# Performance work log

Measured on AMD Instinct MI355X. Metric: run time of the kernel, lower is better.

## Reference

```python
import jax, jax.numpy as jnp
import numpy as np

B, L, H, E, R = 2, 512, 768, 512, 32768
H2 = H // 2


def setup_inputs() -> dict:
    key = jax.random.key(0)
    ks = jax.random.split(key, 16)
    s = 0.02
    inp = {
        "hidden_states": jax.random.normal(ks[0], (B, L, H), dtype=jnp.float32),
        "ent_start": jax.random.randint(ks[1], (B, E), 0, L, dtype=jnp.int32),
        "ent_label": jax.random.randint(ks[2], (B, E), 0, 3, dtype=jnp.int32),
        "rel_head": jax.random.randint(ks[3], (B, R), 0, E, dtype=jnp.int32),
        "rel_tail": jax.random.randint(ks[4], (B, R), 0, E, dtype=jnp.int32),
        "rel_label": jax.random.randint(ks[5], (B, R), 0, 2, dtype=jnp.int32),
        "entity_emb": jax.random.normal(ks[6], (3, H), dtype=jnp.float32) * s,
        "head_W1": jax.random.normal(ks[7], (2 * H, H), dtype=jnp.float32) * s,
        "head_b1": jnp.zeros((H,), dtype=jnp.float32),
        "head_W2": jax.random.normal(ks[8], (H, H2), dtype=jnp.float32) * s,
        "head_b2": jnp.zeros((H2,), dtype=jnp.float32),
        "tail_W1": jax.random.normal(ks[9], (2 * H, H), dtype=jnp.float32) * s,
        "tail_b1": jnp.zeros((H,), dtype=jnp.float32),
        "tail_W2": jax.random.normal(ks[10], (H, H2), dtype=jnp.float32) * s,
        "tail_b2": jnp.zeros((H2,), dtype=jnp.float32),
        "bil_W": jax.random.normal(ks[11], (2, H2, H2), dtype=jnp.float32) * s,
        "lin_W": jax.random.normal(ks[12], (2 * H2, 2), dtype=jnp.float32) * s,
        "lin_b": jnp.zeros((2,), dtype=jnp.float32),
    }
    return inp


def _mlp(x, W1, b1, W2, b2):
    # Linear -> ReLU -> (dropout=identity) -> Linear -> ReLU -> (dropout=identity)
    h = jax.nn.relu(jnp.einsum("brd,dh->brh", x, W1) + b1)
    return jax.nn.relu(jnp.einsum("brh,hk->brk", h, W2) + b2)


def reference(hidden_states, ent_start, ent_label, rel_head, rel_tail, rel_label,
              entity_emb, head_W1, head_b1, head_W2, head_b2,
              tail_W1, tail_b1, tail_W2, tail_b2, bil_W, lin_W, lin_b):
    # Gather entity start token index and label for each relation endpoint
    h_idx = jnp.take_along_axis(ent_start, rel_head, axis=1)  # [B,R]
    t_idx = jnp.take_along_axis(ent_start, rel_tail, axis=1)
    h_lab = jnp.take_along_axis(ent_label, rel_head, axis=1)
    t_lab = jnp.take_along_axis(ent_label, rel_tail, axis=1)

    # Gather hidden states at entity start positions: [B,R,H]
    h_tok = jnp.take_along_axis(hidden_states, h_idx[..., None], axis=1)
    t_tok = jnp.take_along_axis(hidden_states, t_idx[..., None], axis=1)

    head_repr = jnp.concatenate([h_tok, entity_emb[h_lab]], axis=-1)  # [B,R,2H]
    tail_repr = jnp.concatenate([t_tok, entity_emb[t_lab]], axis=-1)

    heads = _mlp(head_repr, head_W1, head_b1, head_W2, head_b2)  # [B,R,H2]
    tails = _mlp(tail_repr, tail_W1, tail_b1, tail_W2, tail_b2)

    # BiaffineAttention: bilinear(x1,x2) + linear(cat(x1,x2))
    bil = jnp.einsum("brd,ode,bre->bro", heads, bil_W, tails)  # [B,R,2]
    lin = jnp.einsum("brc,co->bro", jnp.concatenate([heads, tails], axis=-1), lin_W) + lin_b
    logits = bil + lin  # [B,R,2]

    # Per-doc mean cross-entropy, summed over docs (matches loss accumulation)
    logp = jax.nn.log_softmax(logits, axis=-1)
    ce = -jnp.take_along_axis(logp, rel_label[..., None], axis=-1)[..., 0]  # [B,R]
    loss = ce.mean(axis=-1).sum()

    return loss, logits.reshape(B * R, 2)
```

## Files before the change

kernel.cpp:

```cpp
#include <hip/hip_runtime.h>
#include <math.h>

#define BB 2
#define LL 512
#define HH 768
#define EE 512
#define RR 32768
#define H2 384
#define MM 1024

typedef __attribute__((ext_vector_type(8))) short     bf16x8;
typedef __attribute__((ext_vector_type(4))) float     f32x4;
typedef __attribute__((ext_vector_type(8))) unsigned short u16x8;

#define BUFE (64 * 72)

__device__ __forceinline__ unsigned short f2bf(float f) {
    unsigned int u = __float_as_uint(f);
    u = (u + 0x7FFFu + ((u >> 16) & 1u)) >> 16;
    return (unsigned short)u;
}

__device__ __forceinline__ void wtrans(const float* __restrict__ src,
                                       unsigned short* __restrict__ dst,
                                       int K, int N, int tile, unsigned short* T)
{
    const int t = threadIdx.x;
    const int tn = N >> 5;
    const int n0 = (tile % tn) * 32;
    const int k0 = (tile / tn) * 32;
    const int r  = t >> 3;
    const int c4 = (t & 7) * 4;
    const float4 g = *(const float4*)(src + (size_t)(k0 + r) * N + n0 + c4);
    T[(c4 + 0) * 40 + r] = f2bf(g.x);
    T[(c4 + 1) * 40 + r] = f2bf(g.y);
    T[(c4 + 2) * 40 + r] = f2bf(g.z);
    T[(c4 + 3) * 40 + r] = f2bf(g.w);
    __syncthreads();
    const int n  = t >> 3;
    const int k4 = (t & 7) * 4;
    *(ushort4*)(dst + (size_t)(n0 + n) * K + k0 + k4) = *(ushort4*)&T[n * 40 + k4];
}

__global__ __launch_bounds__(256) void prep(
    const float* __restrict__ hW1, const float* __restrict__ tW1,
    unsigned short* __restrict__ W1ht, unsigned short* __restrict__ W1tt,
    const float* __restrict__ hidden, const int* __restrict__ ent_start,
    const float* __restrict__ emb,
    const float* __restrict__ hb1, const float* __restrict__ tb1,
    unsigned short* __restrict__ Hbf, float* __restrict__ embc,
    float* __restrict__ hlin, float* __restrict__ tlin, float* __restrict__ out)
{
    __shared__ unsigned short T[32 * 40];
    __shared__ float red[4][192];
    const int bid = blockIdx.x;
    const int t = threadIdx.x;

    if (bid == 2200) {
        const float4 z = {0.f, 0.f, 0.f, 0.f};
        ((float4*)hlin)[t] = z; ((float4*)hlin)[256 + t] = z;
        ((float4*)tlin)[t] = z; ((float4*)tlin)[256 + t] = z;
        if (t == 0) out[0] = 0.f;
        return;
    }

    if (bid >= 2176) {
        const int eb = bid - 2176;
        const int tc = t & 63;
        const int kg = t >> 6;
        const int n = eb * 64 + tc;
        const float* W = (n < 768) ? hW1 : tW1;
        const int cc = (n < 768) ? n : n - 768;
        float a0 = 0.f, a1 = 0.f, a2 = 0.f;
        const int kbeg = kg * 192;
        #pragma unroll 8
        for (int k = kbeg; k < kbeg + 192; ++k) {
            const float w = W[(size_t)(768 + k) * 768 + cc];
            a0 += emb[k] * w;
            a1 += emb[768 + k] * w;
            a2 += emb[1536 + k] * w;
        }
        red[kg][0 * 64 + tc] = a0;
        red[kg][1 * 64 + tc] = a1;
        red[kg][2 * 64 + tc] = a2;
        __syncthreads();
        if (kg == 0) {
            const float b = (n < 768) ? hb1[n] : tb1[n - 768];
            #pragma unroll
            for (int l = 0; l < 3; ++l) {
                embc[l * 1536 + n] = b + red[0][l * 64 + tc] + red[1][l * 64 + tc]
                                       + red[2][l * 64 + tc] + red[3][l * 64 + tc];
            }
        }
        return;
    }

    if (bid >= 1152) {
        const int m = bid - 1152;
        if (t >= 96) return;
        const int b = m >> 9;
        const int idx = ent_start[m];
        const float4* s = (const float4*)(hidden + (size_t)(b * LL + idx) * HH);
        const float4 v0 = s[2 * t];
        const float4 v1 = s[2 * t + 1];
        u16x8 o;
        o[0] = f2bf(v0.x); o[1] = f2bf(v0.y); o[2] = f2bf(v0.z); o[3] = f2bf(v0.w);
        o[4] = f2bf(v1.x); o[5] = f2bf(v1.y); o[6] = f2bf(v1.z); o[7] = f2bf(v1.w);
        *(u16x8*)(Hbf + (size_t)m * 768 + 8 * t) = o;
        return;
    }

    if (bid < 576) wtrans(hW1, W1ht, 768, 768, bid, T);
    else           wtrans(tW1, W1tt, 768, 768, bid - 576, T);
}

template<bool RELU, bool BIAS, bool EB, bool WBF16, bool LIN>
__device__ __forceinline__ void gemm_body(
    int tile, int nx,
    const unsigned short* __restrict__ A, int lda, int aoff1,
    const unsigned short* __restrict__ Bt0, const unsigned short* __restrict__ Bt1,
    int ldb, int Nh,
    const float* __restrict__ bias0, const float* __restrict__ bias1,
    const float* __restrict__ embc, const int* __restrict__ labels,
    const float* __restrict__ linW, float* __restrict__ hlin, float* __restrict__ tlin,
    int K, unsigned short* __restrict__ Cb, int ldc,
    unsigned short* As, unsigned short* Bs)
{
    const int tid = threadIdx.x;
    const int n0 = (tile % nx) * 64;
    const int m0 = (tile / nx) * 64;
    const int hf = (n0 >= Nh) ? 1 : 0;
    const unsigned short* Bt = hf ? Bt1 : Bt0;
    const int nc0 = n0 - (hf ? Nh : 0);
    const int aoff = hf ? aoff1 : 0;

    const int sr = tid >> 2;
    const int sk = (tid & 3) * 16;

    const unsigned short* Ap = A + (size_t)(m0 + sr) * lda + aoff + sk;
    const unsigned short* Bp = Bt + (size_t)(nc0 + sr) * ldb + sk;

    const int lane = tid & 63;
    const int wave = tid >> 6;
    const int wm = (wave & 1) * 32;
    const int wn = (wave >> 1) * 32;
    const int l15 = lane & 15;
    const int quad = lane >> 4;
    const int swo = sr * 72 + sk;
    const int aro = quad * 8;

    f32x4 acc00 = {}, acc01 = {}, acc10 = {}, acc11 = {};

    u16x8 pa0, pa1, pb0, pb1;
    u16x8 qa0, qa1, qb0, qb1;

#define GLOADP(ko) { pa0 = *(const u16x8*)(Ap + (ko)); pa1 = *(const u16x8*)(Ap + (ko) + 8); \
                     pb0 = *(const u16x8*)(Bp + (ko)); pb1 = *(const u16x8*)(Bp + (ko) + 8); }
#define GLOADQ(ko) { qa0 = *(const u16x8*)(Ap + (ko)); qa1 = *(const u16x8*)(Ap + (ko) + 8); \
                     qb0 = *(const u16x8*)(Bp + (ko)); qb1 = *(const u16x8*)(Bp + (ko) + 8); }
#define SWRITEP(bi) { unsigned short* Aw = As + (bi) * BUFE; unsigned short* Bw = Bs + (bi) * BUFE; \
                      *(u16x8*)&Aw[swo] = pa0; *(u16x8*)&Aw[swo + 8] = pa1; \
                      *(u16x8*)&Bw[swo] = pb0; *(u16x8*)&Bw[swo + 8] = pb1; }
#define SWRITEQ(bi) { unsigned short* Aw = As + (bi) * BUFE; unsigned short* Bw = Bs + (bi) * BUFE; \
                      *(u16x8*)&Aw[swo] = qa0; *(u16x8*)&Aw[swo + 8] = qa1; \
                      *(u16x8*)&Bw[swo] = qb0; *(u16x8*)&Bw[swo + 8] = qb1; }
#define BAR() { asm volatile("s_waitcnt lgkmcnt(0)" ::: "memory"); \
                __builtin_amdgcn_s_barrier(); \
                __builtin_amdgcn_sched_barrier(0); }
#define MFMA8(bi) { const unsigned short* Ac = As + (bi) * BUFE; \
                    const unsigned short* Bc = Bs + (bi) * BUFE; \
        const bf16x8 fa0 = *(const bf16x8*)&Ac[(wm + l15) * 72 + aro]; \
        const bf16x8 fa1 = *(const bf16x8*)&Ac[(wm + 16 + l15) * 72 + aro]; \
        const bf16x8 fb0 = *(const bf16x8*)&Bc[(wn + l15) * 72 + aro]; \
        const bf16x8 fb1 = *(const bf16x8*)&Bc[(wn + 16 + l15) * 72 + aro]; \
        const bf16x8 ga0 = *(const bf16x8*)&Ac[(wm + l15) * 72 + aro + 32]; \
        const bf16x8 ga1 = *(const bf16x8*)&Ac[(wm + 16 + l15) * 72 + aro + 32]; \
        const bf16x8 gb0 = *(const bf16x8*)&Bc[(wn + l15) * 72 + aro + 32]; \
        const bf16x8 gb1 = *(const bf16x8*)&Bc[(wn + 16 + l15) * 72 + aro + 32]; \
        acc00 = __builtin_amdgcn_mfma_f32_16x16x32_bf16(fa0, fb0, acc00, 0, 0, 0); \
        acc01 = __builtin_amdgcn_mfma_f32_16x16x32_bf16(fa0, fb1, acc01, 0, 0, 0); \
        acc10 = __builtin_amdgcn_mfma_f32_16x16x32_bf16(fa1, fb0, acc10, 0, 0, 0); \
        acc11 = __builtin_amdgcn_mfma_f32_16x16x32_bf16(fa1, fb1, acc11, 0, 0, 0); \
        acc00 = __builtin_amdgcn_mfma_f32_16x16x32_bf16(ga0, gb0, acc00, 0, 0, 0); \
        acc01 = __builtin_amdgcn_mfma_f32_16x16x32_bf16(ga0, gb1, acc01, 0, 0, 0); \
        acc10 = __builtin_amdgcn_mfma_f32_16x16x32_bf16(ga1, gb0, acc10, 0, 0, 0); \
        acc11 = __builtin_amdgcn_mfma_f32_16x16x32_bf16(ga1, gb1, acc11, 0, 0, 0); }

    const int NT = K >> 6;

    GLOADP(0);
    GLOADQ(64);
    SWRITEP(0);

    for (int it = 0; it < NT; it += 2) {
        BAR();
        if (it + 2 < NT) GLOADP((it + 2) << 6);
        MFMA8(0);
        SWRITEQ(1);
        BAR();
        if (it + 3 < NT) GLOADQ((it + 3) << 6);
        MFMA8(1);
        if (it + 2 < NT) SWRITEP(0);
    }

#undef GLOADP
#undef GLOADQ
#undef SWRITEP
#undef SWRITEQ
#undef BAR
#undef MFMA8

    float bias_v0 = 0.f, bias_v1 = 0.f;
    if (BIAS) {
        const float* bb = hf ? bias1 : bias0;
        bias_v0 = bb[nc0 + wn + l15];
        bias_v1 = bb[nc0 + wn + 16 + l15];
    }
    const int col0 = n0 + wn + l15;
    const int col1 = col0 + 16;
    float2 lw0 = {0.f, 0.f}, lw1 = {0.f, 0.f};
    float* lout = nullptr;
    if (LIN) {
        lw0 = ((const float2*)linW)[col0];
        lw1 = ((const float2*)linW)[col1];
        lout = hf ? tlin : hlin;
    }
    const f32x4 accs[2][2] = {{acc00, acc01}, {acc10, acc11}};
    #pragma unroll
    for (int mi = 0; mi < 2; ++mi) {
        #pragma unroll
        for (int r = 0; r < 4; ++r) {
            const int row = m0 + wm + mi * 16 + quad * 4 + r;
            float v0 = accs[mi][0][r];
            float v1 = accs[mi][1][r];
            if (BIAS) { v0 += bias_v0; v1 += bias_v1; }
            if (EB) {
                const int lab = labels[row];
                v0 += embc[lab * 1536 + col0];
                v1 += embc[lab * 1536 + col1];
            }
            if (RELU) { v0 = fmaxf(v0, 0.f); v1 = fmaxf(v1, 0.f); }
            if (WBF16) {
                Cb[(size_t)row * ldc + col0] = f2bf(v0);
                Cb[(size_t)row * ldc + col1] = f2bf(v1);
            }
            if (LIN) {
                float s0 = v0 * lw0.x + v1 * lw1.x;
                float s1 = v0 * lw0.y + v1 * lw1.y;
                #pragma unroll
                for (int o = 8; o >= 1; o >>= 1) {
                    s0 += __shfl_xor(s0, o, 64);
                    s1 += __shfl_xor(s1, o, 64);
                }
                if (l15 == 0) {
                    atomicAdd(&lout[2 * row],     s0);
                    atomicAdd(&lout[2 * row + 1], s1);
                }
            }
        }
    }
}

template<bool RELU, bool BIAS, bool EB, bool WBF16, bool LIN>
__global__ __launch_bounds__(256) void gemm_mfma(
    const unsigned short* __restrict__ A, int lda, int aoff1,
    const unsigned short* __restrict__ Bt0, const unsigned short* __restrict__ Bt1,
    int ldb, int Nh,
    const float* __restrict__ bias0, const float* __restrict__ bias1,
    const float* __restrict__ embc, const int* __restrict__ labels,
    const float* __restrict__ linW, float* __restrict__ hlin, float* __restrict__ tlin,
    int K, unsigned short* __restrict__ Cb, int ldc)
{
    __shared__ __align__(16) unsigned short As[2 * BUFE];
    __shared__ __align__(16) unsigned short Bs[2 * BUFE];
    gemm_body<RELU, BIAS, EB, WBF16, LIN>(
        blockIdx.y * gridDim.x + blockIdx.x, gridDim.x,
        A, lda, aoff1, Bt0, Bt1, ldb, Nh,
        bias0, bias1, embc, labels, linW, hlin, tlin,
        K, Cb, ldc, As, Bs);
}

__global__ __launch_bounds__(256) void gemm1_plus(
    const unsigned short* __restrict__ Hbf,
    const unsigned short* __restrict__ W1ht, const unsigned short* __restrict__ W1tt,
    const float* __restrict__ embc, const int* __restrict__ ent_label,
    unsigned short* __restrict__ Y1bf,
    const float* __restrict__ hW2, const float* __restrict__ tW2,
    const float* __restrict__ bilW,
    unsigned short* __restrict__ W2ht, unsigned short* __restrict__ W2tt,
    unsigned short* __restrict__ bW0t, unsigned short* __restrict__ bW1t,
    const int* __restrict__ rel_head, const int* __restrict__ rel_tail,
    const int* __restrict__ rel_label,
    int* __restrict__ counts2, unsigned* __restrict__ bins)
{
    __shared__ __align__(16) unsigned short As[2 * BUFE];
    __shared__ __align__(16) unsigned short Bs[2 * BUFE];
    const int bid = blockIdx.x;
    if (bid >= 1248) {
        __shared__ int lcnt[128];
        const int tid = threadIdx.x;
        const int blk = bid - 1248;
        const int batch = blk >> 5;
        const int blkb = blk & 31;
        if (tid < 128) lcnt[tid] = 0;
        __syncthreads();
        const int base = blk * 1024;
        #pragma unroll
        for (int k = 0; k < 4; ++k) {
            const int j = base + k * 256 + tid;
            const int h = rel_head[j];
            const int t = rel_tail[j];
            const int lab = rel_label[j];
            const int lbin = ((h >> 6) << 4) | (t >> 5);
            const int slot = atomicAdd(&lcnt[lbin], 1);
            const int gbin = (batch << 7) | lbin;
            bins[(gbin << 10) | (blkb << 5) | slot] =
                (unsigned)j | ((unsigned)lab << 17) |
                ((unsigned)(h & 63) << 18) | ((unsigned)(t & 31) << 24);
        }
        __syncthreads();
        if (tid < 128)
            counts2[(((batch << 7) | tid) << 5) | blkb] = lcnt[tid];
        return;
    }
    if (bid >= 384) {
        const int task = bid - 384;
        if (task < 288)      wtrans(hW2, W2ht, 768, 384, task, As);
        else if (task < 576) wtrans(tW2, W2tt, 768, 384, task - 288, As);
        else if (task < 720) wtrans(bilW, bW0t, 384, 384, task - 576, As);
        else                 wtrans(bilW + 384 * 384, bW1t, 384, 384, task - 720, As);
        return;
    }
    gemm_body<true, false, true, true, false>(
        bid, 24, Hbf, 768, 0, W1ht, W1tt, 768, 768,
        nullptr, nullptr, embc, ent_label, nullptr, nullptr, nullptr,
        768, Y1bf, 1536, As, Bs);
}

__global__ __launch_bounds__(256) void score_rel(
    const unsigned short* __restrict__ hWbf, const unsigned short* __restrict__ HTbf,
    const float* __restrict__ hlin, const float* __restrict__ tlin,
    const float* __restrict__ lin_b,
    const int* __restrict__ counts2, const unsigned* __restrict__ bins,
    float* __restrict__ out)
{
    __shared__ __align__(16) unsigned short As[2][64 * 72];
    __shared__ __align__(16) unsigned short Bs[2][32 * 72];
    __shared__ float wsum[4];
    __shared__ int cbuf[32];

    const int tid = threadIdx.x;
    const int t0 = blockIdx.x * 32;
    const int m0 = blockIdx.y * 64;
    const int batch = m0 >> 9;

    const int asr = tid >> 2;
    const int ask = (tid & 3) * 16;
    const unsigned short* Ap = hWbf + (size_t)(m0 + asr) * 768 + ask;
    const int bsr = tid >> 3;
    const int bsk = (tid & 7) * 8;
    const unsigned short* Bp = HTbf + (size_t)(batch * 512 + t0 + bsr) * 768 + 384 + bsk;

    const int lane = tid & 63;
    const int wave = tid >> 6;
    const int wm = (wave & 1) * 32;
    const int wn = (wave >> 1) * 16;
    const int l15 = lane & 15;
    const int quad = lane >> 4;
    const int aro = quad * 8;
    const int aswo = asr * 72 + ask;
    const int bswo = bsr * 72 + bsk;

    f32x4 p00 = {}, p01 = {};
    f32x4 p10 = {}, p11 = {};

#define KOA(it) (((it) < 6) ? (it) * 64 : ((it) - 6) * 64 + 384)
#define KOB(it) ((((it) < 6) ? (it) : (it) - 6) * 64)

    u16x8 pa0, pa1, pbv;
    u16x8 qa0, qa1, qbv;

#define SGLOADP(it) { pa0 = *(const u16x8*)(Ap + KOA(it)); pa1 = *(const u16x8*)(Ap + KOA(it) + 8); \
                      pbv = *(const u16x8*)(Bp + KOB(it)); }
#define SGLOADQ(it) { qa0 = *(const u16x8*)(Ap + KOA(it)); qa1 = *(const u16x8*)(Ap + KOA(it) + 8); \
                      qbv = *(const u16x8*)(Bp + KOB(it)); }
#define SSWRITEP(bi) { *(u16x8*)&As[bi][aswo] = pa0; *(u16x8*)&As[bi][aswo + 8] = pa1; \
                       *(u16x8*)&Bs[bi][bswo] = pbv; }
#define SSWRITEQ(bi) { *(u16x8*)&As[bi][aswo] = qa0; *(u16x8*)&As[bi][aswo + 8] = qa1; \
                       *(u16x8*)&Bs[bi][bswo] = qbv; }
#define SBAR() { asm volatile("s_waitcnt lgkmcnt(0)" ::: "memory"); \
                 __builtin_amdgcn_s_barrier(); \
                 __builtin_amdgcn_sched_barrier(0); }
#define SMFMA(bi, it) { \
        const unsigned short* Ac = As[bi]; \
        const unsigned short* Bc = Bs[bi]; \
        const bf16x8 fa0 = *(const bf16x8*)&Ac[(wm + l15) * 72 + aro]; \
        const bf16x8 fa1 = *(const bf16x8*)&Ac[(wm + 16 + l15) * 72 + aro]; \
        const bf16x8 fb  = *(const bf16x8*)&Bc[(wn + l15) * 72 + aro]; \
        const bf16x8 ga0 = *(const bf16x8*)&Ac[(wm + l15) * 72 + aro + 32]; \
        const bf16x8 ga1 = *(const bf16x8*)&Ac[(wm + 16 + l15) * 72 + aro + 32]; \
        const bf16x8 gb  = *(const bf16x8*)&Bc[(wn + l15) * 72 + aro + 32]; \
        if ((it) < 6) { \
            p00 = __builtin_amdgcn_mfma_f32_16x16x32_bf16(fa0, fb, p00, 0, 0, 0); \
            p01 = __builtin_amdgcn_mfma_f32_16x16x32_bf16(fa1, fb, p01, 0, 0, 0); \
            p00 = __builtin_amdgcn_mfma_f32_16x16x32_bf16(ga0, gb, p00, 0, 0, 0); \
            p01 = __builtin_amdgcn_mfma_f32_16x16x32_bf16(ga1, gb, p01, 0, 0, 0); \
        } else { \
            p10 = __builtin_amdgcn_mfma_f32_16x16x32_bf16(fa0, fb, p10, 0, 0, 0); \
            p11 = __builtin_amdgcn_mfma_f32_16x16x32_bf16(fa1, fb, p11, 0, 0, 0); \
            p10 = __builtin_amdgcn_mfma_f32_16x16x32_bf16(ga0, gb, p10, 0, 0, 0); \
            p11 = __builtin_amdgcn_mfma_f32_16x16x32_bf16(ga1, gb, p11, 0, 0, 0); \
        } }

    SGLOADP(0);
    SGLOADQ(1);
    SSWRITEP(0);

    #pragma unroll
    for (int it = 0; it < 12; it += 2) {
        SBAR();
        if (it + 2 < 12) SGLOADP(it + 2);
        SMFMA(0, it);
        SSWRITEQ(1);
        SBAR();
        if (it + 3 < 12) SGLOADQ(it + 3);
        SMFMA(1, it + 1);
        if (it + 2 < 12) SSWRITEP(0);
    }

#undef KOA
#undef KOB
#undef SGLOADP
#undef SGLOADQ
#undef SSWRITEP
#undef SSWRITEQ
#undef SBAR
#undef SMFMA

    __syncthreads();
    float* Sl = (float*)&As[0][0];
    const int col = wn + l15;
    #pragma unroll
    for (int mi = 0; mi < 2; ++mi) {
        #pragma unroll
        for (int r = 0; r < 4; ++r) {
            const int row = wm + mi * 16 + quad * 4 + r;
            Sl[row * 33 + col]           = mi ? p01[r] : p00[r];
            Sl[64 * 33 + row * 33 + col] = mi ? p11[r] : p10[r];
        }
    }
    const int bin = (batch << 7) | (((m0 >> 6) & 7) << 4) | (t0 >> 5);
    if (tid < 32) cbuf[tid] = counts2[(bin << 5) | tid];
    __syncthreads();

    const unsigned* mybins = bins + (bin << 10);
    const float lb0 = lin_b[0], lb1 = lin_b[1];
    float ce = 0.f;
    #pragma unroll
    for (int k = 0; k < 4; ++k) {
        const int si = k * 256 + tid;
        const int blkb = si >> 5;
        const int slot = si & 31;
        if (slot < cbuf[blkb]) {
            const unsigned rec = mybins[si];
            const int j   = rec & 0x1FFFF;
            const int lab = (rec >> 17) & 1;
            const int h6  = (rec >> 18) & 63;
            const int t5  = (rec >> 24) & 31;
            const int mh = m0 + h6;
            const int mt = batch * 512 + t0 + t5;
            const float2 hl = ((const float2*)hlin)[mh];
            const float2 tl = ((const float2*)tlin)[mt];
            const int so = h6 * 33 + t5;
            const float z0 = Sl[so]           + hl.x + tl.x + lb0;
            const float z1 = Sl[64 * 33 + so] + hl.y + tl.y + lb1;
            out[1 + 2 * (size_t)j] = z0;
            out[2 + 2 * (size_t)j] = z1;
            const float mx = fmaxf(z0, z1);
            const float mn = fminf(z0, z1);
            ce += mx + log1pf(expf(mn - mx)) - (lab ? z1 : z0);
        }
    }
    #pragma unroll
    for (int o = 32; o >= 1; o >>= 1) ce += __shfl_xor(ce, o, 64);
    if (lane == 0) wsum[wave] = ce;
    __syncthreads();
    if (tid == 0)
        atomicAdd(out, (wsum[0] + wsum[1] + wsum[2] + wsum[3]) * (1.0f / (float)RR));
}

extern "C" void kernel_launch(void* const* d_in, const int* in_sizes, int n_in,
                              void* d_out, int out_size, void* d_ws, size_t ws_size,
                              hipStream_t stream) {
    const float* hidden    = (const float*)d_in[0];
    const int*   ent_start = (const int*)d_in[1];
    const int*   ent_label = (const int*)d_in[2];
    const int*   rel_head  = (const int*)d_in[3];
    const int*   rel_tail  = (const int*)d_in[4];
    const int*   rel_label = (const int*)d_in[5];
    const float* emb       = (const float*)d_in[6];
    const float* head_W1   = (const float*)d_in[7];
    const float* head_b1   = (const float*)d_in[8];
    const float* head_W2   = (const float*)d_in[9];
    const float* head_b2   = (const float*)d_in[10];
    const float* tail_W1   = (const float*)d_in[11];
    const float* tail_b1   = (const float*)d_in[12];
    const float* tail_W2   = (const float*)d_in[13];
    const float* tail_b2   = (const float*)d_in[14];
    const float* bil_W     = (const float*)d_in[15];
    const float* lin_W     = (const float*)d_in[16];
    const float* lin_b     = (const float*)d_in[17];
    float* out = (float*)d_out;

    char* w = (char*)d_ws;
    auto carve = [&](size_t bytes) {
        char* p = w; w += (bytes + 255) & ~(size_t)255; return p;
    };
    unsigned short* Hbf  = (unsigned short*)carve((size_t)MM * 768 * 2);
    unsigned short* Y1bf = (unsigned short*)carve((size_t)MM * 1536 * 2);
    unsigned short* HTbf = (unsigned short*)carve((size_t)MM * 768 * 2);
    unsigned short* hWbf = (unsigned short*)carve((size_t)MM * 768 * 2);
    unsigned short* W1ht = (unsigned short*)carve((size_t)768 * 768 * 2);
    unsigned short* W1tt = (unsigned short*)carve((size_t)768 * 768 * 2);
    unsigned short* W2ht = (unsigned short*)carve((size_t)384 * 768 * 2);
    unsigned short* W2tt = (unsigned short*)carve((size_t)384 * 768 * 2);
    unsigned short* bW0t = (unsigned short*)carve((size_t)384 * 384 * 2);
    unsigned short* bW1t = (unsigned short*)carve((size_t)384 * 384 * 2);
    float*          embc = (float*)carve((size_t)3 * 1536 * 4);
    float*          hlin = (float*)carve(2048 * 4);
    float*          tlin = (float*)carve(2048 * 4);
    int*            counts2 = (int*)carve((size_t)256 * 32 * 4);
    unsigned*       bins = (unsigned*)carve((size_t)256 * 1024 * 4);

    prep<<<2201, 256, 0, stream>>>(
        head_W1, tail_W1, W1ht, W1tt,
        hidden, ent_start, emb, head_b1, tail_b1, Hbf, embc,
        hlin, tlin, out);

    gemm1_plus<<<1312, 256, 0, stream>>>(
        Hbf, W1ht, W1tt, embc, ent_label, Y1bf,
        head_W2, tail_W2, bil_W, W2ht, W2tt, bW0t, bW1t,
        rel_head, rel_tail, rel_label, counts2, bins);

    gemm_mfma<true, true, false, true, true>
        <<<dim3(12, 16), 256, 0, stream>>>(
        Y1bf, 1536, 768, W2ht, W2tt, 768, 384, head_b2, tail_b2,
        nullptr, nullptr, lin_W, hlin, tlin, 768, HTbf, 768);

    gemm_mfma<false, false, false, true, false>
        <<<dim3(12, 16), 256, 0, stream>>>(
        HTbf, 768, 0, bW0t, bW1t, 384, 384, nullptr, nullptr,
        nullptr, nullptr, nullptr, nullptr, nullptr, 384, hWbf, 768);

    score_rel<<<dim3(16, 16), 256, 0, stream>>>(
        hWbf, HTbf, hlin, tlin, lin_b,
        counts2, bins, out);
}
```

Baseline: 143.8 us.

## Fuse weight bf16 conversion and hidden-state gather into GEMM tile loads

```diff
diff --git a/kernel.cpp b/kernel.cpp
--- a/kernel.cpp
+++ b/kernel.cpp
@@ -12,6 +12,7 @@
 typedef __attribute__((ext_vector_type(8))) short     bf16x8;
 typedef __attribute__((ext_vector_type(4))) float     f32x4;
 typedef __attribute__((ext_vector_type(8))) unsigned short u16x8;
+typedef __attribute__((ext_vector_type(4))) unsigned int   u32x4;
 
 #define BUFE (64 * 72)
 
@@ -21,42 +22,24 @@
     return (unsigned short)u;
 }
 
-__device__ __forceinline__ void wtrans(const float* __restrict__ src,
-                                       unsigned short* __restrict__ dst,
-                                       int K, int N, int tile, unsigned short* T)
-{
-    const int t = threadIdx.x;
-    const int tn = N >> 5;
-    const int n0 = (tile % tn) * 32;
-    const int k0 = (tile / tn) * 32;
-    const int r  = t >> 3;
-    const int c4 = (t & 7) * 4;
-    const float4 g = *(const float4*)(src + (size_t)(k0 + r) * N + n0 + c4);
-    T[(c4 + 0) * 40 + r] = f2bf(g.x);
-    T[(c4 + 1) * 40 + r] = f2bf(g.y);
-    T[(c4 + 2) * 40 + r] = f2bf(g.z);
-    T[(c4 + 3) * 40 + r] = f2bf(g.w);
-    __syncthreads();
-    const int n  = t >> 3;
-    const int k4 = (t & 7) * 4;
-    *(ushort4*)(dst + (size_t)(n0 + n) * K + k0 + k4) = *(ushort4*)&T[n * 40 + k4];
+__device__ __forceinline__ unsigned cvt2(float lo, float hi) {
+    unsigned r;
+    asm("v_cvt_pk_bf16_f32 %0, %1, %2" : "=v"(r) : "v"(lo), "v"(hi));
+    return r;
 }
 
 __global__ __launch_bounds__(256) void prep(
     const float* __restrict__ hW1, const float* __restrict__ tW1,
-    unsigned short* __restrict__ W1ht, unsigned short* __restrict__ W1tt,
-    const float* __restrict__ hidden, const int* __restrict__ ent_start,
     const float* __restrict__ emb,
     const float* __restrict__ hb1, const float* __restrict__ tb1,
-    unsigned short* __restrict__ Hbf, float* __restrict__ embc,
+    float* __restrict__ embc,
     float* __restrict__ hlin, float* __restrict__ tlin, float* __restrict__ out)
 {
-    __shared__ unsigned short T[32 * 40];
     __shared__ float red[4][192];
     const int bid = blockIdx.x;
     const int t = threadIdx.x;
 
-    if (bid == 2200) {
+    if (bid == 24) {
         const float4 z = {0.f, 0.f, 0.f, 0.f};
         ((float4*)hlin)[t] = z; ((float4*)hlin)[256 + t] = z;
         ((float4*)tlin)[t] = z; ((float4*)tlin)[256 + t] = z;
@@ -64,62 +47,40 @@
         return;
     }
 
-    if (bid >= 2176) {
-        const int eb = bid - 2176;
-        const int tc = t & 63;
-        const int kg = t >> 6;
-        const int n = eb * 64 + tc;
-        const float* W = (n < 768) ? hW1 : tW1;
-        const int cc = (n < 768) ? n : n - 768;
-        float a0 = 0.f, a1 = 0.f, a2 = 0.f;
-        const int kbeg = kg * 192;
-        #pragma unroll 8
-        for (int k = kbeg; k < kbeg + 192; ++k) {
-            const float w = W[(size_t)(768 + k) * 768 + cc];
-            a0 += emb[k] * w;
-            a1 += emb[768 + k] * w;
-            a2 += emb[1536 + k] * w;
+    const int tc = t & 63;
+    const int kg = t >> 6;
+    const int n = bid * 64 + tc;
+    const float* W = (n < 768) ? hW1 : tW1;
+    const int cc = (n < 768) ? n : n - 768;
+    float a0 = 0.f, a1 = 0.f, a2 = 0.f;
+    const int kbeg = kg * 192;
+    #pragma unroll 8
+    for (int k = kbeg; k < kbeg + 192; ++k) {
+        const float w = W[(size_t)(768 + k) * 768 + cc];
+        a0 += emb[k] * w;
+        a1 += emb[768 + k] * w;
+        a2 += emb[1536 + k] * w;
+    }
+    red[kg][0 * 64 + tc] = a0;
+    red[kg][1 * 64 + tc] = a1;
+    red[kg][2 * 64 + tc] = a2;
+    __syncthreads();
+    if (kg == 0) {
+        const float b = (n < 768) ? hb1[n] : tb1[n - 768];
+        #pragma unroll
+        for (int l = 0; l < 3; ++l) {
+            embc[l * 1536 + n] = b + red[0][l * 64 + tc] + red[1][l * 64 + tc]
+                                   + red[2][l * 64 + tc] + red[3][l * 64 + tc];
         }
-        red[kg][0 * 64 + tc] = a0;
-        red[kg][1 * 64 + tc] = a1;
-        red[kg][2 * 64 + tc] = a2;
-        __syncthreads();
-        if (kg == 0) {
-            const float b = (n < 768) ? hb1[n] : tb1[n - 768];
-            #pragma unroll
-            for (int l = 0; l < 3; ++l) {
-                embc[l * 1536 + n] = b + red[0][l * 64 + tc] + red[1][l * 64 + tc]
-                                       + red[2][l * 64 + tc] + red[3][l * 64 + tc];
-            }
-        }
-        return;
-    }
-
-    if (bid >= 1152) {
-        const int m = bid - 1152;
-        if (t >= 96) return;
-        const int b = m >> 9;
-        const int idx = ent_start[m];
-        const float4* s = (const float4*)(hidden + (size_t)(b * LL + idx) * HH);
-        const float4 v0 = s[2 * t];
-        const float4 v1 = s[2 * t + 1];
-        u16x8 o;
-        o[0] = f2bf(v0.x); o[1] = f2bf(v0.y); o[2] = f2bf(v0.z); o[3] = f2bf(v0.w);
-        o[4] = f2bf(v1.x); o[5] = f2bf(v1.y); o[6] = f2bf(v1.z); o[7] = f2bf(v1.w);
-        *(u16x8*)(Hbf + (size_t)m * 768 + 8 * t) = o;
-        return;
-    }
-
-    if (bid < 576) wtrans(hW1, W1ht, 768, 768, bid, T);
-    else           wtrans(tW1, W1tt, 768, 768, bid - 576, T);
-}
-
-template<bool RELU, bool BIAS, bool EB, bool WBF16, bool LIN>
+    }
+}
+
+template<bool GATHER, bool RELU, bool BIAS, bool EB, bool LIN>
 __device__ __forceinline__ void gemm_body(
     int tile, int nx,
-    const unsigned short* __restrict__ A, int lda, int aoff1,
-    const unsigned short* __restrict__ Bt0, const unsigned short* __restrict__ Bt1,
-    int ldb, int Nh,
+    const unsigned short* __restrict__ Abf, int lda, int aoff1,
+    const float* __restrict__ hidden, const int* __restrict__ ent_start,
+    const float* __restrict__ Wf0, const float* __restrict__ Wf1, int ldN, int Nh,
     const float* __restrict__ bias0, const float* __restrict__ bias1,
     const float* __restrict__ embc, const int* __restrict__ labels,
     const float* __restrict__ linW, float* __restrict__ hlin, float* __restrict__ tlin,
@@ -130,15 +91,24 @@
     const int n0 = (tile % nx) * 64;
     const int m0 = (tile / nx) * 64;
     const int hf = (n0 >= Nh) ? 1 : 0;
-    const unsigned short* Bt = hf ? Bt1 : Bt0;
     const int nc0 = n0 - (hf ? Nh : 0);
-    const int aoff = hf ? aoff1 : 0;
 
     const int sr = tid >> 2;
     const int sk = (tid & 3) * 16;
-
-    const unsigned short* Ap = A + (size_t)(m0 + sr) * lda + aoff + sk;
-    const unsigned short* Bp = Bt + (size_t)(nc0 + sr) * ldb + sk;
+    const unsigned short* ApH = nullptr;
+    const float* ApF = nullptr;
+    if constexpr (GATHER) {
+        const int m = m0 + sr;
+        const int b = m >> 9;
+        const int idx = ent_start[m];
+        ApF = hidden + (size_t)(b * LL + idx) * HH + sk;
+    } else {
+        ApH = Abf + (size_t)(m0 + sr) * lda + (hf ? aoff1 : 0) + sk;
+    }
+
+    const int kk = (tid >> 4) * 4;
+    const int nn = (tid & 15) * 4;
+    const float* BpF = (hf ? Wf1 : Wf0) + (size_t)kk * ldN + nc0 + nn;
 
     const int lane = tid & 63;
     const int wave = tid >> 6;
@@ -151,19 +121,66 @@
 
     f32x4 acc00 = {}, acc01 = {}, acc10 = {}, acc11 = {};
 
-    u16x8 pa0, pa1, pb0, pb1;
-    u16x8 qa0, qa1, qb0, qb1;
-
-#define GLOADP(ko) { pa0 = *(const u16x8*)(Ap + (ko)); pa1 = *(const u16x8*)(Ap + (ko) + 8); \
-                     pb0 = *(const u16x8*)(Bp + (ko)); pb1 = *(const u16x8*)(Bp + (ko) + 8); }
-#define GLOADQ(ko) { qa0 = *(const u16x8*)(Ap + (ko)); qa1 = *(const u16x8*)(Ap + (ko) + 8); \
-                     qb0 = *(const u16x8*)(Bp + (ko)); qb1 = *(const u16x8*)(Bp + (ko) + 8); }
-#define SWRITEP(bi) { unsigned short* Aw = As + (bi) * BUFE; unsigned short* Bw = Bs + (bi) * BUFE; \
-                      *(u16x8*)&Aw[swo] = pa0; *(u16x8*)&Aw[swo + 8] = pa1; \
-                      *(u16x8*)&Bw[swo] = pb0; *(u16x8*)&Bw[swo + 8] = pb1; }
-#define SWRITEQ(bi) { unsigned short* Aw = As + (bi) * BUFE; unsigned short* Bw = Bs + (bi) * BUFE; \
-                      *(u16x8*)&Aw[swo] = qa0; *(u16x8*)&Aw[swo + 8] = qa1; \
-                      *(u16x8*)&Bw[swo] = qb0; *(u16x8*)&Bw[swo + 8] = qb1; }
+    u16x8 pH0, pH1, qH0, qH1;
+    float4 pA0, pA1, pA2, pA3, qA0, qA1, qA2, qA3;
+    float4 pB0, pB1, pB2, pB3, qB0, qB1, qB2, qB3;
+
+#define GLOADP(ko) { \
+    if constexpr (GATHER) { \
+        pA0 = *(const float4*)(ApF + (ko));      pA1 = *(const float4*)(ApF + (ko) + 4); \
+        pA2 = *(const float4*)(ApF + (ko) + 8);  pA3 = *(const float4*)(ApF + (ko) + 12); \
+    } else { \
+        pH0 = *(const u16x8*)(ApH + (ko)); pH1 = *(const u16x8*)(ApH + (ko) + 8); \
+    } \
+    pB0 = *(const float4*)(BpF + (size_t)((ko) + 0) * ldN); \
+    pB1 = *(const float4*)(BpF + (size_t)((ko) + 1) * ldN); \
+    pB2 = *(const float4*)(BpF + (size_t)((ko) + 2) * ldN); \
+    pB3 = *(const float4*)(BpF + (size_t)((ko) + 3) * ldN); }
+#define GLOADQ(ko) { \
+    if constexpr (GATHER) { \
+        qA0 = *(const float4*)(ApF + (ko));      qA1 = *(const float4*)(ApF + (ko) + 4); \
+        qA2 = *(const float4*)(ApF + (ko) + 8);  qA3 = *(const float4*)(ApF + (ko) + 12); \
+    } else { \
+        qH0 = *(const u16x8*)(ApH + (ko)); qH1 = *(const u16x8*)(ApH + (ko) + 8); \
+    } \
+    qB0 = *(const float4*)(BpF + (size_t)((ko) + 0) * ldN); \
+    qB1 = *(const float4*)(BpF + (size_t)((ko) + 1) * ldN); \
+    qB2 = *(const float4*)(BpF + (size_t)((ko) + 2) * ldN); \
+    qB3 = *(const float4*)(BpF + (size_t)((ko) + 3) * ldN); }
+#define SWRITEP(bi) { \
+    unsigned short* Aw = As + (bi) * BUFE; unsigned short* Bw = Bs + (bi) * BUFE; \
+    if constexpr (GATHER) { \
+        u32x4 av; \
+        av.x = cvt2(pA0.x, pA0.y); av.y = cvt2(pA0.z, pA0.w); \
+        av.z = cvt2(pA1.x, pA1.y); av.w = cvt2(pA1.z, pA1.w); \
+        *(u32x4*)&Aw[swo] = av; \
+        av.x = cvt2(pA2.x, pA2.y); av.y = cvt2(pA2.z, pA2.w); \
+        av.z = cvt2(pA3.x, pA3.y); av.w = cvt2(pA3.z, pA3.w); \
+        *(u32x4*)&Aw[swo + 8] = av; \
+    } else { \
+        *(u16x8*)&Aw[swo] = pH0; *(u16x8*)&Aw[swo + 8] = pH1; \
+    } \
+    *(uint2*)&Bw[(nn + 0) * 72 + kk] = make_uint2(cvt2(pB0.x, pB1.x), cvt2(pB2.x, pB3.x)); \
+    *(uint2*)&Bw[(nn + 1) * 72 + kk] = make_uint2(cvt2(pB0.y, pB1.y), cvt2(pB2.y, pB3.y)); \
+    *(uint2*)&Bw[(nn + 2) * 72 + kk] = make_uint2(cvt2(pB0.z, pB1.z), cvt2(pB2.z, pB3.z)); \
+    *(uint2*)&Bw[(nn + 3) * 72 + kk] = make_uint2(cvt2(pB0.w, pB1.w), cvt2(pB2.w, pB3.w)); }
+#define SWRITEQ(bi) { \
+    unsigned short* Aw = As + (bi) * BUFE; unsigned short* Bw = Bs + (bi) * BUFE; \
+    if constexpr (GATHER) { \
+        u32x4 av; \
+        av.x = cvt2(qA0.x, qA0.y); av.y = cvt2(qA0.z, qA0.w); \
+        av.z = cvt2(qA1.x, qA1.y); av.w = cvt2(qA1.z, qA1.w); \
+        *(u32x4*)&Aw[swo] = av; \
+        av.x = cvt2(qA2.x, qA2.y); av.y = cvt2(qA2.z, qA2.w); \
+        av.z = cvt2(qA3.x, qA3.y); av.w = cvt2(qA3.z, qA3.w); \
+        *(u32x4*)&Aw[swo + 8] = av; \
+    } else { \
+        *(u16x8*)&Aw[swo] = qH0; *(u16x8*)&Aw[swo + 8] = qH1; \
+    } \
+    *(uint2*)&Bw[(nn + 0) * 72 + kk] = make_uint2(cvt2(qB0.x, qB1.x), cvt2(qB2.x, qB3.x)); \
+    *(uint2*)&Bw[(nn + 1) * 72 + kk] = make_uint2(cvt2(qB0.y, qB1.y), cvt2(qB2.y, qB3.y)); \
+    *(uint2*)&Bw[(nn + 2) * 72 + kk] = make_uint2(cvt2(qB0.z, qB1.z), cvt2(qB2.z, qB3.z)); \
+    *(uint2*)&Bw[(nn + 3) * 72 + kk] = make_uint2(cvt2(qB0.w, qB1.w), cvt2(qB2.w, qB3.w)); }
 #define BAR() { asm volatile("s_waitcnt lgkmcnt(0)" ::: "memory"); \
                 __builtin_amdgcn_s_barrier(); \
                 __builtin_amdgcn_sched_barrier(0); }
@@ -240,10 +257,8 @@
                 v1 += embc[lab * 1536 + col1];
             }
             if (RELU) { v0 = fmaxf(v0, 0.f); v1 = fmaxf(v1, 0.f); }
-            if (WBF16) {
-                Cb[(size_t)row * ldc + col0] = f2bf(v0);
-                Cb[(size_t)row * ldc + col1] = f2bf(v1);
-            }
+            Cb[(size_t)row * ldc + col0] = f2bf(v0);
+            Cb[(size_t)row * ldc + col1] = f2bf(v1);
             if (LIN) {
                 float s0 = v0 * lw0.x + v1 * lw1.x;
                 float s1 = v0 * lw0.y + v1 * lw1.y;
@@ -261,34 +276,29 @@
     }
 }
 
-template<bool RELU, bool BIAS, bool EB, bool WBF16, bool LIN>
+template<bool RELU, bool BIAS, bool LIN>
 __global__ __launch_bounds__(256) void gemm_mfma(
     const unsigned short* __restrict__ A, int lda, int aoff1,
-    const unsigned short* __restrict__ Bt0, const unsigned short* __restrict__ Bt1,
-    int ldb, int Nh,
+    const float* __restrict__ Wf0, const float* __restrict__ Wf1, int ldN, int Nh,
     const float* __restrict__ bias0, const float* __restrict__ bias1,
-    const float* __restrict__ embc, const int* __restrict__ labels,
     const float* __restrict__ linW, float* __restrict__ hlin, float* __restrict__ tlin,
     int K, unsigned short* __restrict__ Cb, int ldc)
 {
     __shared__ __align__(16) unsigned short As[2 * BUFE];
     __shared__ __align__(16) unsigned short Bs[2 * BUFE];
-    gemm_body<RELU, BIAS, EB, WBF16, LIN>(
+    gemm_body<false, RELU, BIAS, false, LIN>(
         blockIdx.y * gridDim.x + blockIdx.x, gridDim.x,
-        A, lda, aoff1, Bt0, Bt1, ldb, Nh,
-        bias0, bias1, embc, labels, linW, hlin, tlin,
+        A, lda, aoff1, nullptr, nullptr,
+        Wf0, Wf1, ldN, Nh,
+        bias0, bias1, nullptr, nullptr, linW, hlin, tlin,
         K, Cb, ldc, As, Bs);
 }
 
 __global__ __launch_bounds__(256) void gemm1_plus(
-    const unsigned short* __restrict__ Hbf,
-    const unsigned short* __restrict__ W1ht, const unsigned short* __restrict__ W1tt,
+    const float* __restrict__ hidden, const int* __restrict__ ent_start,
+    const float* __restrict__ hW1, const float* __restrict__ tW1,
     const float* __restrict__ embc, const int* __restrict__ ent_label,
     unsigned short* __restrict__ Y1bf,
-    const float* __restrict__ hW2, const float* __restrict__ tW2,
-    const float* __restrict__ bilW,
-    unsigned short* __restrict__ W2ht, unsigned short* __restrict__ W2tt,
-    unsigned short* __restrict__ bW0t, unsigned short* __restrict__ bW1t,
     const int* __restrict__ rel_head, const int* __restrict__ rel_tail,
     const int* __restrict__ rel_label,
     int* __restrict__ counts2, unsigned* __restrict__ bins)
@@ -296,10 +306,10 @@
     __shared__ __align__(16) unsigned short As[2 * BUFE];
     __shared__ __align__(16) unsigned short Bs[2 * BUFE];
     const int bid = blockIdx.x;
-    if (bid >= 1248) {
+    if (bid >= 384) {
         __shared__ int lcnt[128];
         const int tid = threadIdx.x;
-        const int blk = bid - 1248;
+        const int blk = bid - 384;
         const int batch = blk >> 5;
         const int blkb = blk & 31;
         if (tid < 128) lcnt[tid] = 0;
@@ -323,16 +333,9 @@
             counts2[(((batch << 7) | tid) << 5) | blkb] = lcnt[tid];
         return;
     }
-    if (bid >= 384) {
-        const int task = bid - 384;
-        if (task < 288)      wtrans(hW2, W2ht, 768, 384, task, As);
-        else if (task < 576) wtrans(tW2, W2tt, 768, 384, task - 288, As);
-        else if (task < 720) wtrans(bilW, bW0t, 384, 384, task - 576, As);
-        else                 wtrans(bilW + 384 * 384, bW1t, 384, 384, task - 720, As);
-        return;
-    }
-    gemm_body<true, false, true, true, false>(
-        bid, 24, Hbf, 768, 0, W1ht, W1tt, 768, 768,
+    gemm_body<true, true, false, true, false>(
+        bid, 24, nullptr, 0, 0, hidden, ent_start,
+        hW1, tW1, 768, 768,
         nullptr, nullptr, embc, ent_label, nullptr, nullptr, nullptr,
         768, Y1bf, 1536, As, Bs);
 }
@@ -516,41 +519,29 @@
     auto carve = [&](size_t bytes) {
         char* p = w; w += (bytes + 255) & ~(size_t)255; return p;
     };
-    unsigned short* Hbf  = (unsigned short*)carve((size_t)MM * 768 * 2);
     unsigned short* Y1bf = (unsigned short*)carve((size_t)MM * 1536 * 2);
     unsigned short* HTbf = (unsigned short*)carve((size_t)MM * 768 * 2);
     unsigned short* hWbf = (unsigned short*)carve((size_t)MM * 768 * 2);
-    unsigned short* W1ht = (unsigned short*)carve((size_t)768 * 768 * 2);
-    unsigned short* W1tt = (unsigned short*)carve((size_t)768 * 768 * 2);
-    unsigned short* W2ht = (unsigned short*)carve((size_t)384 * 768 * 2);
-    unsigned short* W2tt = (unsigned short*)carve((size_t)384 * 768 * 2);
-    unsigned short* bW0t = (unsigned short*)carve((size_t)384 * 384 * 2);
-    unsigned short* bW1t = (unsigned short*)carve((size_t)384 * 384 * 2);
     float*          embc = (float*)carve((size_t)3 * 1536 * 4);
     float*          hlin = (float*)carve(2048 * 4);
     float*          tlin = (float*)carve(2048 * 4);
     int*            counts2 = (int*)carve((size_t)256 * 32 * 4);
     unsigned*       bins = (unsigned*)carve((size_t)256 * 1024 * 4);
 
-    prep<<<2201, 256, 0, stream>>>(
-        head_W1, tail_W1, W1ht, W1tt,
-        hidden, ent_start, emb, head_b1, tail_b1, Hbf, embc,
-        hlin, tlin, out);
-
-    gemm1_plus<<<1312, 256, 0, stream>>>(
-        Hbf, W1ht, W1tt, embc, ent_label, Y1bf,
-        head_W2, tail_W2, bil_W, W2ht, W2tt, bW0t, bW1t,
+    prep<<<25, 256, 0, stream>>>(
+        head_W1, tail_W1, emb, head_b1, tail_b1, embc, hlin, tlin, out);
+
+    gemm1_plus<<<448, 256, 0, stream>>>(
+        hidden, ent_start, head_W1, tail_W1, embc, ent_label, Y1bf,
         rel_head, rel_tail, rel_label, counts2, bins);
 
-    gemm_mfma<true, true, false, true, true>
-        <<<dim3(12, 16), 256, 0, stream>>>(
-        Y1bf, 1536, 768, W2ht, W2tt, 768, 384, head_b2, tail_b2,
-        nullptr, nullptr, lin_W, hlin, tlin, 768, HTbf, 768);
-
-    gemm_mfma<false, false, false, true, false>
-        <<<dim3(12, 16), 256, 0, stream>>>(
-        HTbf, 768, 0, bW0t, bW1t, 384, 384, nullptr, nullptr,
-        nullptr, nullptr, nullptr, nullptr, nullptr, 384, hWbf, 768);
+    gemm_mfma<true, true, true><<<dim3(12, 16), 256, 0, stream>>>(
+        Y1bf, 1536, 768, head_W2, tail_W2, 384, 384, head_b2, tail_b2,
+        lin_W, hlin, tlin, 768, HTbf, 768);
+
+    gemm_mfma<false, false, false><<<dim3(12, 16), 256, 0, stream>>>(
+        HTbf, 768, 0, bil_W, bil_W + 384 * 384, 384, 384, nullptr, nullptr,
+        nullptr, nullptr, nullptr, 384, hWbf, 768);
 
     score_rel<<<dim3(16, 16), 256, 0, stream>>>(
         hWbf, HTbf, hlin, tlin, lin_b,
```

After: 153.6 us. 1.07x slower.
